# Optimization experiments

Hardware: AMD Instinct MI355X
Metric: run time of the kernel (lower is better)

The kernel has to match this reference:

```python
import jax, jax.numpy as jnp
import numpy as np
import math

CHI, CHO, UP = 256, 128, 2
KH = KW = 3


def bilinear_up_kernel(k):
    f = math.ceil(k / 2)
    c = (2 * f - 1 - f % 2) / (2.0 * f)
    w = np.zeros((k, k), dtype=np.float32)
    for i in range(k):
        for j in range(k):
            w[i, j] = (1 - abs(i / f - c)) * (1 - abs(j / f - c))
    return w


def setup_inputs() -> dict:
    key = jax.random.key(0)
    ks = jax.random.split(key, 8)
    x = jax.random.normal(ks[0], (8, CHI, 64, 64), dtype=jnp.float32)
    # DCNv2 weights
    w_dcn = jax.random.normal(ks[1], (CHO, CHI, KH, KW), dtype=jnp.float32) * 0.02
    b_dcn = jnp.zeros((CHO,), dtype=jnp.float32)
    # offset/mask conv: out channels = 3*KH*KW (2*9 offsets + 9 mask), zero-init as in DCNv2
    w_off = jnp.zeros((3 * KH * KW, CHI, KH, KW), dtype=jnp.float32)
    b_off = jnp.zeros((3 * KH * KW,), dtype=jnp.float32)
    # BatchNorm (eval math) params
    bn_gamma = jax.random.uniform(ks[2], (CHO,), dtype=jnp.float32, minval=0.5, maxval=1.5)
    bn_beta = jax.random.normal(ks[3], (CHO,), dtype=jnp.float32) * 0.1
    bn_mean = jax.random.normal(ks[4], (CHO,), dtype=jnp.float32) * 0.1
    bn_var = jax.random.uniform(ks[5], (CHO,), dtype=jnp.float32, minval=0.5, maxval=1.5)
    # fixed bilinear depthwise transpose-conv weights [CHO,1,2r,2r]
    w_up = jnp.broadcast_to(jnp.asarray(bilinear_up_kernel(UP * 2)), (CHO, 1, UP * 2, UP * 2)).astype(jnp.float32)
    # 1x1 conv to 1 channel
    w_1x1 = jax.random.normal(ks[6], (1, CHO, 1, 1), dtype=jnp.float32) * 0.05
    return dict(x=x, w_dcn=w_dcn, b_dcn=b_dcn, w_off=w_off, b_off=b_off,
                bn_gamma=bn_gamma, bn_beta=bn_beta, bn_mean=bn_mean, bn_var=bn_var,
                w_up=w_up, w_1x1=w_1x1)


def conv2d(x, w, b=None, stride=1, pad=1):
    y = jax.lax.conv_general_dilated(x, w, (stride, stride), [(pad, pad), (pad, pad)],
                                     dimension_numbers=('NCHW', 'OIHW', 'NCHW'))
    if b is not None:
        y = y + b[None, :, None, None]
    return y


def bilinear_sample(img, py, px):
    # img: [C,H,W]; py,px: [P] float coords. Zero padding outside.
    C, H, W = img.shape
    y0 = jnp.floor(py); x0 = jnp.floor(px)
    y1 = y0 + 1; x1 = x0 + 1
    wy1 = py - y0; wy0 = 1.0 - wy1
    wx1 = px - x0; wx0 = 1.0 - wx1

    def gather(yi, xi):
        valid = (yi >= 0) & (yi < H) & (xi >= 0) & (xi < W)
        yc = jnp.clip(yi, 0, H - 1).astype(jnp.int32)
        xc = jnp.clip(xi, 0, W - 1).astype(jnp.int32)
        v = img[:, yc, xc]  # [C,P]
        return v * valid.astype(img.dtype)[None, :]

    out = (gather(y0, x0) * (wy0 * wx0)[None, :] + gather(y0, x1) * (wy0 * wx1)[None, :]
           + gather(y1, x0) * (wy1 * wx0)[None, :] + gather(y1, x1) * (wy1 * wx1)[None, :])
    return out  # [C,P]


def dcn_v2(x, w, b, offset, mask):
    # x: [B,Ci,H,W]; offset: [B,2*K,H,W]; mask: [B,K,H,W]; K=9; stride 1, pad 1.
    B, Ci, H, W = x.shape
    K = KH * KW
    # base sampling grid per kernel tap
    ky, kx = jnp.meshgrid(jnp.arange(KH) - 1, jnp.arange(KW) - 1, indexing='ij')  # [3,3]
    oy, ox = jnp.meshgrid(jnp.arange(H), jnp.arange(W), indexing='ij')  # [H,W]
    base_y = oy[None, :, :] + ky.reshape(K, 1, 1)  # [K,H,W]
    base_x = ox[None, :, :] + kx.reshape(K, 1, 1)

    off = offset.reshape(B, K, 2, H, W)
    py = base_y[None] + off[:, :, 0]  # [B,K,H,W]
    px = base_x[None] + off[:, :, 1]

    def per_sample(img, py_b, px_b, m_b):
        samp = bilinear_sample(img, py_b.reshape(-1), px_b.reshape(-1))  # [Ci, K*H*W]
        samp = samp.reshape(Ci, K, H, W) * m_b[None]  # [Ci,K,H,W]
        # conv accumulate: w [Co,Ci,KH,KW] -> [Co,Ci,K]
        return jnp.einsum('cik,ikhw->chw', w.reshape(w.shape[0], Ci, K), samp[None].swapaxes(0, 1).squeeze(1)[None].squeeze(0)[None].squeeze(0).reshape(Ci, K, H, W))

    def per_sample2(img, py_b, px_b, m_b):
        samp = bilinear_sample(img, py_b.reshape(-1), px_b.reshape(-1)).reshape(Ci, K, H, W)
        samp = samp * m_b[None]
        return jnp.einsum('oik,ikhw->ohw', w.reshape(w.shape[0], Ci, K), samp)

    y = jax.vmap(per_sample2)(x, py, px, mask)  # [B,Co,H,W]
    return y + b[None, :, None, None]


def reference(x, w_dcn, b_dcn, w_off, b_off, bn_gamma, bn_beta, bn_mean, bn_var, w_up, w_1x1):
    K = KH * KW
    om = conv2d(x, w_off, b_off, stride=1, pad=1)  # [B,3K,H,W]
    o1, o2, m = om[:, :K], om[:, K:2 * K], om[:, 2 * K:]
    # DCNv2 ordering: offsets interleaved as (dy,dx) per tap -> o1=dy, o2=dx
    offset = jnp.concatenate([o1[:, :, None], o2[:, :, None]], axis=2).reshape(x.shape[0], 2 * K, x.shape[2], x.shape[3])
    mask = jax.nn.sigmoid(m)
    y = dcn_v2(x, w_dcn, b_dcn, offset, mask)
    # BN (eval) + ReLU
    inv = jax.lax.rsqrt(bn_var + 1e-5)
    y = jax.nn.relu((y - bn_mean[None, :, None, None]) * (bn_gamma * inv)[None, :, None, None] + bn_beta[None, :, None, None])
    # depthwise transpose conv, kernel 2r, stride r, pad r//2
    r = UP
    y = jax.lax.conv_transpose(y, w_up.transpose(2, 3, 1, 0),  # HWIO with I=1 (feature_group_count)
                               strides=(r, r), padding=[(r // 2, r // 2), (r // 2, r // 2)],
                               dimension_numbers=('NCHW', 'HWIO', 'NCHW'),
                               transpose_kernel=True)
    # NOTE: jax.lax.conv_transpose lacks groups; emulate depthwise via per-channel trick below instead.
    return y


def depthwise_conv_transpose(y, w_up, r):
    # y: [B,C,H,W]; w_up: [C,1,k,k]; equivalent to input-dilated conv with flipped kernel
    C = y.shape[1]
    k = w_up.shape[2]
    wf = w_up[:, :, ::-1, ::-1]  # flip for transpose conv
    pad = k - 1 - r // 2
    return jax.lax.conv_general_dilated(y, wf, window_strides=(1, 1),
                                        padding=[(pad, pad), (pad, pad)],
                                        lhs_dilation=(r, r),
                                        dimension_numbers=('NCHW', 'OIHW', 'NCHW'),
                                        feature_group_count=C)


def reference(x, w_dcn, b_dcn, w_off, b_off, bn_gamma, bn_beta, bn_mean, bn_var, w_up, w_1x1):
    K = KH * KW
    om = conv2d(x, w_off, b_off, stride=1, pad=1)
    o1, o2, m = om[:, :K], om[:, K:2 * K], om[:, 2 * K:]
    offset = jnp.concatenate([o1[:, :, None], o2[:, :, None]], axis=2).reshape(x.shape[0], 2 * K, x.shape[2], x.shape[3])
    mask = jax.nn.sigmoid(m)
    y = dcn_v2(x, w_dcn, b_dcn, offset, mask)
    inv = jax.lax.rsqrt(bn_var + 1e-5)
    y = jax.nn.relu((y - bn_mean[None, :, None, None]) * (bn_gamma * inv)[None, :, None, None] + bn_beta[None, :, None, None])
    y = depthwise_conv_transpose(y, w_up, UP)  # [B,CHO,2H,2W]
    y = conv2d(y, w_1x1, None, stride=1, pad=0)  # [B,1,2H,2W]
    return jax.nn.sigmoid(y)
```

## Files before the change

kernel.cpp:

```cpp
#include <hip/hip_runtime.h>
#include <math.h>

typedef __attribute__((ext_vector_type(8))) short short8;
typedef __attribute__((ext_vector_type(4))) float floatx4;

__device__ __forceinline__ unsigned short bf16r(float f) {
  union { float f; unsigned int u; } v; v.f = f;
  unsigned int u = v.u;
  return (unsigned short)((u + 0x7fffu + ((u >> 16) & 1u)) >> 16);
}
__device__ __forceinline__ unsigned int bf16h(float f) {
  union { float f; unsigned int u; } v; v.f = f;
  return (v.u + 0x8000u) >> 16;
}
__device__ __forceinline__ float bf2f(unsigned int u) {
  union { unsigned int u; float f; } v; v.u = u << 16; return v.f;
}
__device__ __forceinline__ void glds16(const void* g, void* l) {
  __builtin_amdgcn_global_load_lds(
      (const __attribute__((address_space(1))) unsigned int*)g,
      (__attribute__((address_space(3))) unsigned int*)l, 16, 0, 0);
}

__global__ __launch_bounds__(256) void k_pre(
    const float* __restrict__ x,
    const float* __restrict__ w_dcn, const float* __restrict__ w_off,
    const float* __restrict__ b_dcn,
    const float* __restrict__ bn_g, const float* __restrict__ bn_b,
    const float* __restrict__ bn_m, const float* __restrict__ bn_v,
    const float* __restrict__ w_up, const float* __restrict__ w1x1,
    unsigned short* __restrict__ xT,
    unsigned short* __restrict__ wt_dcn, unsigned short* __restrict__ wt_off,
    float* __restrict__ vtab, float* __restrict__ bntab,
    unsigned int* __restrict__ offflags) {
  __shared__ unsigned short sx[32 * 264];
  int e = blockIdx.x * 256 + threadIdx.x;
  if (e < 294912) {
    int s = e >> 12;
    int r = e & 4095;
    int ot = r >> 9;
    int lane = (r >> 3) & 63;
    int j = e & 7;
    int l15 = lane & 15, quad = lane >> 4;
    int o = ot * 16 + l15;
    int k = s % 9, cg = s / 9;
    int c = cg * 32 + quad * 8 + j;
    wt_dcn[e] = bf16r(w_dcn[(o * 256 + c) * 9 + k]);
  }
  bool nz = false;
  if (e < 73728) {
    int cg = e / 9216;
    int r = e % 9216;
    int frag = r >> 9;
    int k = frag >> 1, ot = frag & 1;
    int lane = (r >> 3) & 63, j = e & 7;
    int l15 = lane & 15, quad = lane >> 4;
    int oc = ot * 16 + l15;
    int c = cg * 32 + quad * 8 + j;
    float wv = (oc < 27) ? w_off[(oc * 256 + c) * 9 + k] : 0.f;
    wt_off[e] = bf16r(wv);
    nz = (wv != 0.f);
  }
  unsigned long long ba = __ballot(nz);
  if (blockIdx.x < 288 && (threadIdx.x & 63) == 0)
    offflags[blockIdx.x * 4 + (threadIdx.x >> 6)] = (ba != 0ull) ? 1u : 0u;
  if (e < 2048) {
    int o = e >> 4;
    vtab[e] = w1x1[o] * w_up[e];
  }
  if (e < 128) {
    float g = bn_g[e] * rsqrtf(bn_v[e] + 1e-5f);
    bntab[e] = g;
    bntab[128 + e] = (b_dcn[e] - bn_m[e]) * g + bn_b[e];
  }
  if (blockIdx.x < 1024) {
    int b = blockIdx.x & 7, px0 = ((blockIdx.x >> 3) & 127) * 32;
    int t = threadIdx.x;
    int px = t & 31, cg = t >> 5;
    const float* xsrc = x + (((size_t)(b * 256 + cg * 32)) << 12) + px0 + px;
#pragma unroll
    for (int cc = 0; cc < 32; ++cc)
      sx[px * 264 + cg * 32 + cc] = bf16r(xsrc[(size_t)cc << 12]);
    __syncthreads();
#pragma unroll
    for (int j = 0; j < 4; ++j) {
      int unit = t + j * 256;
      int p = unit >> 5, chunk = unit & 31;
      uint4 v = *(const uint4*)&sx[p * 264 + chunk * 8];
      *(uint4*)&xT[((size_t)((b << 12) + px0 + p)) * 256 + chunk * 8] = v;
    }
  }
}

__global__ __launch_bounds__(256, 2) void k_dcn(
    const unsigned short* __restrict__ xT, const unsigned short* __restrict__ wt,
    const unsigned short* __restrict__ wtoff, const float* __restrict__ b_off,
    const float* __restrict__ vtab, const float* __restrict__ bntab,
    const unsigned int* __restrict__ offflags, float* __restrict__ R) {
  int b = blockIdx.x & 7, row = blockIdx.x >> 3;
  __shared__ unsigned short sW[2 * 12288];
  __shared__ ushort4 s_ti[576];
  __shared__ float4 s_tw[576];
  __shared__ unsigned int s_fl[4];
  int t = threadIdx.x, lane = t & 63, wvx = t >> 6;
  int l15 = lane & 15, quad = lane >> 4;
  int px = wvx * 16 + l15;
  const unsigned short* xb = xT + (((size_t)b) << 12) * 256;
  const short8 zz = {0, 0, 0, 0, 0, 0, 0, 0};
  unsigned short* som = (unsigned short*)s_ti;

  {
    unsigned int a = 0;
    for (int i = t; i < 1152; i += 256) a |= offflags[i];
    a = __any(a != 0u) ? 1u : 0u;
    if (lane == 0) s_fl[wvx] = a;
  }
  __syncthreads();
  const bool offnz = (s_fl[0] | s_fl[1] | s_fl[2] | s_fl[3]) != 0u;

  if (offnz) {
    int pixk[9]; bool vkk[9];
#pragma unroll
    for (int k = 0; k < 9; ++k) {
      int yy = row + k / 3 - 1, xx = px + k % 3 - 1;
      vkk[k] = ((unsigned)yy < 64u) & ((unsigned)xx < 64u);
      pixk[k] = vkk[k] ? (yy * 64 + xx) : 0;
    }
    floatx4 oacc[2];
    oacc[0] = (floatx4){0.f, 0.f, 0.f, 0.f};
    oacc[1] = (floatx4){0.f, 0.f, 0.f, 0.f};

#pragma unroll
    for (int i = 0; i < 5; ++i) {
      int frag = wvx + i * 4;
      if (frag < 18)
        glds16(wtoff + (size_t)frag * 512 + lane * 8, &sW[frag * 512]);
    }
    __syncthreads();

    for (int cg = 0; cg < 8; ++cg) {
      unsigned short* buf = sW + (cg & 1) * 9216;
      int cb = cg * 32 + quad * 8;
      short8 bx[9];
#pragma unroll
      for (int k = 0; k < 9; ++k) {
        short8 v = *(const short8*)&xb[(size_t)pixk[k] * 256 + cb];
        bx[k] = vkk[k] ? v : zz;
      }
      if (cg < 7) {
        const unsigned short* wsrc = wtoff + (size_t)(cg + 1) * 9216;
        unsigned short* nbuf = sW + ((cg + 1) & 1) * 9216;
#pragma unroll
        for (int i = 0; i < 5; ++i) {
          int frag = wvx + i * 4;
          if (frag < 18)
            glds16(wsrc + (size_t)frag * 512 + lane * 8, &nbuf[frag * 512]);
        }
      }
#pragma unroll
      for (int k = 0; k < 9; ++k) {
        short8 a0 = *(const short8*)&buf[(k * 2 + 0) * 512 + lane * 8];
        short8 a1 = *(const short8*)&buf[(k * 2 + 1) * 512 + lane * 8];
        oacc[0] = __builtin_amdgcn_mfma_f32_16x16x32_bf16(a0, bx[k], oacc[0], 0, 0, 0);
        oacc[1] = __builtin_amdgcn_mfma_f32_16x16x32_bf16(a1, bx[k], oacc[1], 0, 0, 0);
      }
      __syncthreads();
    }
#pragma unroll
    for (int ot = 0; ot < 2; ++ot)
#pragma unroll
      for (int r = 0; r < 4; ++r) {
        int o = ot * 16 + quad * 4 + r;
        if (o < 27) som[o * 64 + px] = bf16r(oacc[ot][r] + b_off[o]);
      }
    __syncthreads();
  }

  {
    float to1[3], to2[3], tmv[3];
    if (offnz) {
#pragma unroll
      for (int ii = 0; ii < 3; ++ii) {
        int i = t + ii * 256;
        if (i < 576) {
          int k = i >> 6, p = i & 63;
          to1[ii] = bf2f(som[k * 64 + p]);
          to2[ii] = bf2f(som[(9 + k) * 64 + p]);
          tmv[ii] = bf2f(som[(18 + k) * 64 + p]);
        }
      }
      __syncthreads();
    } else {
#pragma unroll
      for (int ii = 0; ii < 3; ++ii) {
        int i = t + ii * 256;
        if (i < 576) {
          int k = i >> 6;
          to1[ii] = bf2f(bf16r(b_off[k]));
          to2[ii] = bf2f(bf16r(b_off[9 + k]));
          tmv[ii] = bf2f(bf16r(b_off[18 + k]));
        }
      }
    }
#pragma unroll
    for (int ii = 0; ii < 3; ++ii) {
      int i = t + ii * 256;
      if (i < 576) {
        int k = i >> 6, p = i & 63;
        float m = 1.f / (1.f + __expf(-tmv[ii]));
        float py = (float)(row + k / 3 - 1) + to1[ii];
        float pxf = (float)(p + (k % 3) - 1) + to2[ii];
        float fy = floorf(py), fx = floorf(pxf);
        int iy = (int)fy, ix = (int)fx;
        float wy1 = py - fy, wy0 = 1.f - wy1;
        float wx1 = pxf - fx, wx0 = 1.f - wx1;
        bool y0ok = (iy >= 0) & (iy < 64), y1ok = (iy >= -1) & (iy < 63);
        bool x0ok = (ix >= 0) & (ix < 64), x1ok = (ix >= -1) & (ix < 63);
        int iy0 = min(max(iy, 0), 63), iy1 = min(max(iy + 1, 0), 63);
        int ix0 = min(max(ix, 0), 63), ix1 = min(max(ix + 1, 0), 63);
        s_ti[i] = make_ushort4((unsigned short)(iy0 * 64 + ix0), (unsigned short)(iy0 * 64 + ix1),
                               (unsigned short)(iy1 * 64 + ix0), (unsigned short)(iy1 * 64 + ix1));
        float4 w;
        w.x = (y0ok && x0ok) ? m * wy0 * wx0 : 0.f;
        w.y = (y0ok && x1ok) ? m * wy0 * wx1 : 0.f;
        w.z = (y1ok && x0ok) ? m * wy1 * wx0 : 0.f;
        w.w = (y1ok && x1ok) ? m * wy1 * wx1 : 0.f;
        s_tw[i] = w;
      }
    }
  }
  __syncthreads();

  const uint4 z4 = make_uint4(0u, 0u, 0u, 0u);

  floatx4 acc[8];
#pragma unroll
  for (int i = 0; i < 8; ++i) acc[i] = (floatx4){0.f, 0.f, 0.f, 0.f};

  uint4 traw[12];
  {
    int cbase = quad * 8;
#pragma unroll
    for (int kk = 0; kk < 3; ++kk) {
      ushort4 ti = s_ti[(kk << 6) + px];
      float4 twn = s_tw[(kk << 6) + px];
      uint4 t0 = z4, t1 = z4, t2 = z4, t3 = z4;
      if (__any(twn.x != 0.f)) t0 = *(const uint4*)&xb[(size_t)ti.x * 256 + cbase];
      if (__any(twn.y != 0.f)) t1 = *(const uint4*)&xb[(size_t)ti.y * 256 + cbase];
      if (__any(twn.z != 0.f)) t2 = *(const uint4*)&xb[(size_t)ti.z * 256 + cbase];
      if (__any(twn.w != 0.f)) t3 = *(const uint4*)&xb[(size_t)ti.w * 256 + cbase];
      traw[kk * 4 + 0] = t0; traw[kk * 4 + 1] = t1;
      traw[kk * 4 + 2] = t2; traw[kk * 4 + 3] = t3;
    }
  }
  {
    const unsigned short* wsrc = wt;
#pragma unroll
    for (int i = 0; i < 6; ++i) {
      int blk = wvx * 6 + i;
      glds16(wsrc + (size_t)blk * 512 + lane * 8, &sW[blk * 512]);
    }
  }
  __syncthreads();

  int lofs = lane * 8;

  for (int phase = 0; phase < 24; ++phase) {
    unsigned short* buf = sW + (phase & 1) * 12288;
    unsigned short* nbuf = sW + ((phase + 1) & 1) * 12288;
    if (phase < 23) {
      const unsigned short* wsrc = wt + (size_t)(phase + 1) * 12288;
#pragma unroll
      for (int i = 0; i < 6; ++i) {
        int blk = wvx * 6 + i;
        glds16(wsrc + (size_t)blk * 512 + lane * 8, &nbuf[blk * 512]);
      }
    }
    int nphase = phase + 1;
    int ncbase = (nphase / 3) * 32 + quad * 8;

#pragma unroll
    for (int kk = 0; kk < 3; ++kk) {
      int k = (phase % 3) * 3 + kk;
      float4 tw = s_tw[(k << 6) + px];
      union { uint4 u; short8 s; } x0, x1, x2, x3;
      x0.u = traw[kk * 4 + 0]; x1.u = traw[kk * 4 + 1];
      x2.u = traw[kk * 4 + 2]; x3.u = traw[kk * 4 + 3];
      if (phase < 23) {
        int nk = (nphase % 3) * 3 + kk;
        ushort4 ti = s_ti[(nk << 6) + px];
        float4 twn = s_tw[(nk << 6) + px];
        uint4 t0 = z4, t1 = z4, t2 = z4, t3 = z4;
        if (__any(twn.x != 0.f)) t0 = *(const uint4*)&xb[(size_t)ti.x * 256 + ncbase];
        if (__any(twn.y != 0.f)) t1 = *(const uint4*)&xb[(size_t)ti.y * 256 + ncbase];
        if (__any(twn.z != 0.f)) t2 = *(const uint4*)&xb[(size_t)ti.z * 256 + ncbase];
        if (__any(twn.w != 0.f)) t3 = *(const uint4*)&xb[(size_t)ti.w * 256 + ncbase];
        traw[kk * 4 + 0] = t0; traw[kk * 4 + 1] = t1;
        traw[kk * 4 + 2] = t2; traw[kk * 4 + 3] = t3;
      }
      float r[8];
#pragma unroll
      for (int j = 0; j < 8; ++j) r[j] = tw.x * bf2f((unsigned short)x0.s[j]);
      if (__any(tw.y != 0.f)) {
#pragma unroll
        for (int j = 0; j < 8; ++j) r[j] += tw.y * bf2f((unsigned short)x1.s[j]);
      }
      if (__any(tw.z != 0.f)) {
#pragma unroll
        for (int j = 0; j < 8; ++j) r[j] += tw.z * bf2f((unsigned short)x2.s[j]);
      }
      if (__any(tw.w != 0.f)) {
#pragma unroll
        for (int j = 0; j < 8; ++j) r[j] += tw.w * bf2f((unsigned short)x3.s[j]);
      }
      union { uint4 u; short8 s; } bu;
      bu.u = make_uint4(bf16h(r[0]) | (bf16h(r[1]) << 16), bf16h(r[2]) | (bf16h(r[3]) << 16),
                        bf16h(r[4]) | (bf16h(r[5]) << 16), bf16h(r[6]) | (bf16h(r[7]) << 16));
      const unsigned short* bk = buf + kk * 4096 + lofs;
#pragma unroll
      for (int ot = 0; ot < 8; ++ot) {
        short8 af = *(const short8*)&bk[ot * 512];
        acc[ot] = __builtin_amdgcn_mfma_f32_16x16x32_bf16(af, bu.s, acc[ot], 0, 0, 0);
      }
    }
    __syncthreads();
  }

  float* sv = (float*)sW;
  float* sbn = sv + 2176;
  for (int i = t; i < 2048; i += 256) sv[(i >> 4) * 17 + (i & 15)] = vtab[i];
  if (t < 256) sbn[t] = bntab[t];
  __syncthreads();

  float rpart[16];
#pragma unroll
  for (int i = 0; i < 16; ++i) rpart[i] = 0.f;
#pragma unroll
  for (int ot = 0; ot < 8; ++ot)
#pragma unroll
    for (int r = 0; r < 4; ++r) {
      int o = ot * 16 + quad * 4 + r;
      float yv = fmaxf(acc[ot][r] * sbn[o] + sbn[128 + o], 0.f);
      const float* vp = &sv[o * 17];
#pragma unroll
      for (int tt = 0; tt < 16; ++tt) rpart[tt] += vp[tt] * yv;
    }
#pragma unroll
  for (int tt = 0; tt < 16; ++tt) {
    rpart[tt] += __shfl_xor(rpart[tt], 16, 64);
    rpart[tt] += __shfl_xor(rpart[tt], 32, 64);
  }
#pragma unroll
  for (int j = 0; j < 4; ++j) {
    int slot = quad * 4 + j;
    R[(((size_t)(b * 16 + slot)) << 12) + row * 64 + px] = rpart[slot];
  }
}

__global__ __launch_bounds__(256) void k_upb(
    const float* __restrict__ R, float* __restrict__ out) {
  int b = blockIdx.x & 7, sub = blockIdx.x >> 3;
  int inner = sub * 256 + threadIdx.x;
  int X = inner & 127, Y = inner >> 7;
  int i0, wu0, wu1, j0, wv0, wv1;
  if (Y & 1) { i0 = (Y - 1) >> 1; wu0 = 2; wu1 = 0; }
  else       { i0 = (Y - 2) / 2;  wu0 = 3; wu1 = 1; }
  if (X & 1) { j0 = (X - 1) >> 1; wv0 = 2; wv1 = 0; }
  else       { j0 = (X - 2) / 2;  wv0 = 3; wv1 = 1; }
  int i1 = i0 + 1, j1 = j0 + 1;
  float mi0 = ((unsigned)i0 < 64u) ? 1.f : 0.f;
  float mi1 = ((unsigned)i1 < 64u) ? 1.f : 0.f;
  float mj0 = ((unsigned)j0 < 64u) ? 1.f : 0.f;
  float mj1 = ((unsigned)j1 < 64u) ? 1.f : 0.f;
  int i0c = min(max(i0, 0), 63), i1c = min(max(i1, 0), 63);
  int j0c = min(max(j0, 0), 63), j1c = min(max(j1, 0), 63);
  const float* Rb = R + (((size_t)b) << 16);
  float s = mi0 * mj0 * Rb[((wu0 * 4 + wv0) << 12) + (i0c << 6) + j0c] +
            mi0 * mj1 * Rb[((wu0 * 4 + wv1) << 12) + (i0c << 6) + j1c] +
            mi1 * mj0 * Rb[((wu1 * 4 + wv0) << 12) + (i1c << 6) + j0c] +
            mi1 * mj1 * Rb[((wu1 * 4 + wv1) << 12) + (i1c << 6) + j1c];
  out[(b << 14) + inner] = 1.f / (1.f + __expf(-s));
}

extern "C" void kernel_launch(void* const* d_in, const int* in_sizes, int n_in,
                              void* d_out, int out_size, void* d_ws, size_t ws_size,
                              hipStream_t stream) {
  const float* x        = (const float*)d_in[0];
  const float* w_dcn    = (const float*)d_in[1];
  const float* b_dcn    = (const float*)d_in[2];
  const float* w_off    = (const float*)d_in[3];
  const float* b_off    = (const float*)d_in[4];
  const float* bn_gamma = (const float*)d_in[5];
  const float* bn_beta  = (const float*)d_in[6];
  const float* bn_mean  = (const float*)d_in[7];
  const float* bn_var   = (const float*)d_in[8];
  const float* w_up     = (const float*)d_in[9];
  const float* w_1x1    = (const float*)d_in[10];
  float* out = (float*)d_out;

  float* ws = (float*)d_ws;
  unsigned short* xT     = (unsigned short*)ws;
  unsigned short* wt_dcn = (unsigned short*)(ws + 4194304);
  unsigned short* wt_off = (unsigned short*)(ws + 4341760);
  float* vtab            = ws + 4378624;
  float* bntab           = ws + 4380672;
  unsigned int* offflags = (unsigned int*)(ws + 4380928);
  float* R               = ws + 4823296;

  k_pre<<<1152, 256, 0, stream>>>(x, w_dcn, w_off, b_dcn, bn_gamma, bn_beta,
                                  bn_mean, bn_var, w_up, w_1x1,
                                  xT, wt_dcn, wt_off, vtab, bntab, offflags);
  k_dcn<<<512, 256, 0, stream>>>(xT, wt_dcn, wt_off, b_off, vtab, bntab,
                                 offflags, R);
  k_upb<<<512, 256, 0, stream>>>(R, out);
}
```

Before: 146.4 us.

## Process two output rows per 512-thread block to share DCN weight tiles

The DCN kernel now launches 256 blocks of 512 threads, each covering two image rows, instead of 512 blocks of 256 threads covering one row. Each phase's weight tile streamed into LDS is reused across both rows, which halves weight traffic per output row. The sampling index and weight tables now stay in per-thread registers instead of shared memory, removing that LDS round trip and one barrier. When offsets are all zero, the kernel also issues dummy loads of the neighbouring input rows to warm the cache. The costs are higher register pressure from 9 extra float4/ushort4 values per thread and only one block per CU, so less room to hide latency.

```diff
diff --git a/kernel.cpp b/kernel.cpp
--- a/kernel.cpp
+++ b/kernel.cpp
@@ -92,33 +92,46 @@
   }
 }
 
-__global__ __launch_bounds__(256, 2) void k_dcn(
+__global__ __launch_bounds__(512, 2) void k_dcn(
     const unsigned short* __restrict__ xT, const unsigned short* __restrict__ wt,
     const unsigned short* __restrict__ wtoff, const float* __restrict__ b_off,
     const float* __restrict__ vtab, const float* __restrict__ bntab,
     const unsigned int* __restrict__ offflags, float* __restrict__ R) {
-  int b = blockIdx.x & 7, row = blockIdx.x >> 3;
+  int b = blockIdx.x & 7, row0 = (blockIdx.x >> 3) * 2;
   __shared__ unsigned short sW[2 * 12288];
-  __shared__ ushort4 s_ti[576];
-  __shared__ float4 s_tw[576];
-  __shared__ unsigned int s_fl[4];
+  __shared__ unsigned int s_fl[8];
   int t = threadIdx.x, lane = t & 63, wvx = t >> 6;
   int l15 = lane & 15, quad = lane >> 4;
-  int px = wvx * 16 + l15;
+  int row_local = wvx >> 2, wv4 = wvx & 3;
+  int row = row0 + row_local;
+  int px = wv4 * 16 + l15;
   const unsigned short* xb = xT + (((size_t)b) << 12) * 256;
   const short8 zz = {0, 0, 0, 0, 0, 0, 0, 0};
-  unsigned short* som = (unsigned short*)s_ti;
+  unsigned short* som = (unsigned short*)sW + 18432;
 
   {
     unsigned int a = 0;
-    for (int i = t; i < 1152; i += 256) a |= offflags[i];
+    for (int i = t; i < 1152; i += 512) a |= offflags[i];
     a = __any(a != 0u) ? 1u : 0u;
     if (lane == 0) s_fl[wvx] = a;
   }
   __syncthreads();
-  const bool offnz = (s_fl[0] | s_fl[1] | s_fl[2] | s_fl[3]) != 0u;
-
-  if (offnz) {
+  unsigned int fl = 0;
+#pragma unroll
+  for (int i = 0; i < 8; ++i) fl |= s_fl[i];
+  const bool offnz = fl != 0u;
+
+  if (!offnz) {
+    int wr0 = max(row0 - 1, 0), wr1 = min(row0 + 2, 63);
+    for (int rr = wr0; rr <= wr1; ++rr) {
+      const uint4* src = (const uint4*)(xb + ((size_t)(rr << 6)) * 256);
+#pragma unroll
+      for (int i = 0; i < 4; ++i) {
+        uint4 v = src[t + (i << 9)];
+        asm volatile("" :: "v"(v.x), "v"(v.y), "v"(v.z), "v"(v.w));
+      }
+    }
+  } else {
     int pixk[9]; bool vkk[9];
 #pragma unroll
     for (int k = 0; k < 9; ++k) {
@@ -129,15 +142,13 @@
     floatx4 oacc[2];
     oacc[0] = (floatx4){0.f, 0.f, 0.f, 0.f};
     oacc[1] = (floatx4){0.f, 0.f, 0.f, 0.f};
-
-#pragma unroll
-    for (int i = 0; i < 5; ++i) {
-      int frag = wvx + i * 4;
+#pragma unroll
+    for (int i = 0; i < 3; ++i) {
+      int frag = wvx + i * 8;
       if (frag < 18)
         glds16(wtoff + (size_t)frag * 512 + lane * 8, &sW[frag * 512]);
     }
     __syncthreads();
-
     for (int cg = 0; cg < 8; ++cg) {
       unsigned short* buf = sW + (cg & 1) * 9216;
       int cb = cg * 32 + quad * 8;
@@ -151,8 +162,8 @@
         const unsigned short* wsrc = wtoff + (size_t)(cg + 1) * 9216;
         unsigned short* nbuf = sW + ((cg + 1) & 1) * 9216;
 #pragma unroll
-        for (int i = 0; i < 5; ++i) {
-          int frag = wvx + i * 4;
+        for (int i = 0; i < 3; ++i) {
+          int frag = wvx + i * 8;
           if (frag < 18)
             glds16(wsrc + (size_t)frag * 512 + lane * 8, &nbuf[frag * 512]);
         }
@@ -171,68 +182,49 @@
 #pragma unroll
       for (int r = 0; r < 4; ++r) {
         int o = ot * 16 + quad * 4 + r;
-        if (o < 27) som[o * 64 + px] = bf16r(oacc[ot][r] + b_off[o]);
+        if (o < 27) som[row_local * 1728 + o * 64 + px] = bf16r(oacc[ot][r] + b_off[o]);
       }
     __syncthreads();
   }
 
+  ushort4 tir[9]; float4 twr[9];
   {
-    float to1[3], to2[3], tmv[3];
-    if (offnz) {
-#pragma unroll
-      for (int ii = 0; ii < 3; ++ii) {
-        int i = t + ii * 256;
-        if (i < 576) {
-          int k = i >> 6, p = i & 63;
-          to1[ii] = bf2f(som[k * 64 + p]);
-          to2[ii] = bf2f(som[(9 + k) * 64 + p]);
-          tmv[ii] = bf2f(som[(18 + k) * 64 + p]);
-        }
-      }
-      __syncthreads();
-    } else {
-#pragma unroll
-      for (int ii = 0; ii < 3; ++ii) {
-        int i = t + ii * 256;
-        if (i < 576) {
-          int k = i >> 6;
-          to1[ii] = bf2f(bf16r(b_off[k]));
-          to2[ii] = bf2f(bf16r(b_off[9 + k]));
-          tmv[ii] = bf2f(bf16r(b_off[18 + k]));
-        }
-      }
-    }
-#pragma unroll
-    for (int ii = 0; ii < 3; ++ii) {
-      int i = t + ii * 256;
-      if (i < 576) {
-        int k = i >> 6, p = i & 63;
-        float m = 1.f / (1.f + __expf(-tmv[ii]));
-        float py = (float)(row + k / 3 - 1) + to1[ii];
-        float pxf = (float)(p + (k % 3) - 1) + to2[ii];
-        float fy = floorf(py), fx = floorf(pxf);
-        int iy = (int)fy, ix = (int)fx;
-        float wy1 = py - fy, wy0 = 1.f - wy1;
-        float wx1 = pxf - fx, wx0 = 1.f - wx1;
-        bool y0ok = (iy >= 0) & (iy < 64), y1ok = (iy >= -1) & (iy < 63);
-        bool x0ok = (ix >= 0) & (ix < 64), x1ok = (ix >= -1) & (ix < 63);
-        int iy0 = min(max(iy, 0), 63), iy1 = min(max(iy + 1, 0), 63);
-        int ix0 = min(max(ix, 0), 63), ix1 = min(max(ix + 1, 0), 63);
-        s_ti[i] = make_ushort4((unsigned short)(iy0 * 64 + ix0), (unsigned short)(iy0 * 64 + ix1),
-                               (unsigned short)(iy1 * 64 + ix0), (unsigned short)(iy1 * 64 + ix1));
-        float4 w;
-        w.x = (y0ok && x0ok) ? m * wy0 * wx0 : 0.f;
-        w.y = (y0ok && x1ok) ? m * wy0 * wx1 : 0.f;
-        w.z = (y1ok && x0ok) ? m * wy1 * wx0 : 0.f;
-        w.w = (y1ok && x1ok) ? m * wy1 * wx1 : 0.f;
-        s_tw[i] = w;
-      }
-    }
-  }
-  __syncthreads();
+    const unsigned short* smr = som + row_local * 1728;
+#pragma unroll
+    for (int k = 0; k < 9; ++k) {
+      float o1, o2, mv;
+      if (offnz) {
+        o1 = bf2f(smr[k * 64 + px]);
+        o2 = bf2f(smr[(9 + k) * 64 + px]);
+        mv = bf2f(smr[(18 + k) * 64 + px]);
+      } else {
+        o1 = bf2f(bf16r(b_off[k]));
+        o2 = bf2f(bf16r(b_off[9 + k]));
+        mv = bf2f(bf16r(b_off[18 + k]));
+      }
+      float m = 1.f / (1.f + __expf(-mv));
+      float py = (float)(row + k / 3 - 1) + o1;
+      float pxf = (float)(px + (k % 3) - 1) + o2;
+      float fy = floorf(py), fx = floorf(pxf);
+      int iy = (int)fy, ix = (int)fx;
+      float wy1 = py - fy, wy0 = 1.f - wy1;
+      float wx1 = pxf - fx, wx0 = 1.f - wx1;
+      bool y0ok = (iy >= 0) & (iy < 64), y1ok = (iy >= -1) & (iy < 63);
+      bool x0ok = (ix >= 0) & (ix < 64), x1ok = (ix >= -1) & (ix < 63);
+      int iy0 = min(max(iy, 0), 63), iy1 = min(max(iy + 1, 0), 63);
+      int ix0 = min(max(ix, 0), 63), ix1 = min(max(ix + 1, 0), 63);
+      tir[k] = make_ushort4((unsigned short)(iy0 * 64 + ix0), (unsigned short)(iy0 * 64 + ix1),
+                            (unsigned short)(iy1 * 64 + ix0), (unsigned short)(iy1 * 64 + ix1));
+      float4 w;
+      w.x = (y0ok && x0ok) ? m * wy0 * wx0 : 0.f;
+      w.y = (y0ok && x1ok) ? m * wy0 * wx1 : 0.f;
+      w.z = (y1ok && x0ok) ? m * wy1 * wx0 : 0.f;
+      w.w = (y1ok && x1ok) ? m * wy1 * wx1 : 0.f;
+      twr[k] = w;
+    }
+  }
 
   const uint4 z4 = make_uint4(0u, 0u, 0u, 0u);
-
   floatx4 acc[8];
 #pragma unroll
   for (int i = 0; i < 8; ++i) acc[i] = (floatx4){0.f, 0.f, 0.f, 0.f};
@@ -242,8 +234,7 @@
     int cbase = quad * 8;
 #pragma unroll
     for (int kk = 0; kk < 3; ++kk) {
-      ushort4 ti = s_ti[(kk << 6) + px];
-      float4 twn = s_tw[(kk << 6) + px];
+      ushort4 ti = tir[kk]; float4 twn = twr[kk];
       uint4 t0 = z4, t1 = z4, t2 = z4, t3 = z4;
       if (__any(twn.x != 0.f)) t0 = *(const uint4*)&xb[(size_t)ti.x * 256 + cbase];
       if (__any(twn.y != 0.f)) t1 = *(const uint4*)&xb[(size_t)ti.y * 256 + cbase];
@@ -254,81 +245,82 @@
     }
   }
   {
-    const unsigned short* wsrc = wt;
-#pragma unroll
-    for (int i = 0; i < 6; ++i) {
-      int blk = wvx * 6 + i;
-      glds16(wsrc + (size_t)blk * 512 + lane * 8, &sW[blk * 512]);
+#pragma unroll
+    for (int i = 0; i < 3; ++i) {
+      int blk = wvx * 3 + i;
+      glds16(wt + (size_t)blk * 512 + lane * 8, &sW[blk * 512]);
     }
   }
   __syncthreads();
 
-  int lofs = lane * 8;
-
-  for (int phase = 0; phase < 24; ++phase) {
-    unsigned short* buf = sW + (phase & 1) * 12288;
-    unsigned short* nbuf = sW + ((phase + 1) & 1) * 12288;
-    if (phase < 23) {
-      const unsigned short* wsrc = wt + (size_t)(phase + 1) * 12288;
-#pragma unroll
-      for (int i = 0; i < 6; ++i) {
-        int blk = wvx * 6 + i;
-        glds16(wsrc + (size_t)blk * 512 + lane * 8, &nbuf[blk * 512]);
-      }
-    }
-    int nphase = phase + 1;
-    int ncbase = (nphase / 3) * 32 + quad * 8;
-
-#pragma unroll
-    for (int kk = 0; kk < 3; ++kk) {
-      int k = (phase % 3) * 3 + kk;
-      float4 tw = s_tw[(k << 6) + px];
-      union { uint4 u; short8 s; } x0, x1, x2, x3;
-      x0.u = traw[kk * 4 + 0]; x1.u = traw[kk * 4 + 1];
-      x2.u = traw[kk * 4 + 2]; x3.u = traw[kk * 4 + 3];
-      if (phase < 23) {
-        int nk = (nphase % 3) * 3 + kk;
-        ushort4 ti = s_ti[(nk << 6) + px];
-        float4 twn = s_tw[(nk << 6) + px];
-        uint4 t0 = z4, t1 = z4, t2 = z4, t3 = z4;
-        if (__any(twn.x != 0.f)) t0 = *(const uint4*)&xb[(size_t)ti.x * 256 + ncbase];
-        if (__any(twn.y != 0.f)) t1 = *(const uint4*)&xb[(size_t)ti.y * 256 + ncbase];
-        if (__any(twn.z != 0.f)) t2 = *(const uint4*)&xb[(size_t)ti.z * 256 + ncbase];
-        if (__any(twn.w != 0.f)) t3 = *(const uint4*)&xb[(size_t)ti.w * 256 + ncbase];
-        traw[kk * 4 + 0] = t0; traw[kk * 4 + 1] = t1;
-        traw[kk * 4 + 2] = t2; traw[kk * 4 + 3] = t3;
-      }
-      float r[8];
-#pragma unroll
-      for (int j = 0; j < 8; ++j) r[j] = tw.x * bf2f((unsigned short)x0.s[j]);
-      if (__any(tw.y != 0.f)) {
-#pragma unroll
-        for (int j = 0; j < 8; ++j) r[j] += tw.y * bf2f((unsigned short)x1.s[j]);
-      }
-      if (__any(tw.z != 0.f)) {
-#pragma unroll
-        for (int j = 0; j < 8; ++j) r[j] += tw.z * bf2f((unsigned short)x2.s[j]);
-      }
-      if (__any(tw.w != 0.f)) {
-#pragma unroll
-        for (int j = 0; j < 8; ++j) r[j] += tw.w * bf2f((unsigned short)x3.s[j]);
-      }
-      union { uint4 u; short8 s; } bu;
-      bu.u = make_uint4(bf16h(r[0]) | (bf16h(r[1]) << 16), bf16h(r[2]) | (bf16h(r[3]) << 16),
-                        bf16h(r[4]) | (bf16h(r[5]) << 16), bf16h(r[6]) | (bf16h(r[7]) << 16));
-      const unsigned short* bk = buf + kk * 4096 + lofs;
-#pragma unroll
-      for (int ot = 0; ot < 8; ++ot) {
-        short8 af = *(const short8*)&bk[ot * 512];
-        acc[ot] = __builtin_amdgcn_mfma_f32_16x16x32_bf16(af, bu.s, acc[ot], 0, 0, 0);
-      }
-    }
-    __syncthreads();
+  for (int p3 = 0; p3 < 8; ++p3) {
+#pragma unroll
+    for (int sub = 0; sub < 3; ++sub) {
+      int phase = p3 * 3 + sub;
+      unsigned short* buf = sW + (phase & 1) * 12288;
+      unsigned short* nbuf = sW + ((phase + 1) & 1) * 12288;
+      bool notlast = (sub < 2) | (p3 < 7);
+      if (notlast) {
+        const unsigned short* wsrc = wt + (size_t)(phase + 1) * 12288;
+#pragma unroll
+        for (int i = 0; i < 3; ++i) {
+          int blk = wvx * 3 + i;
+          glds16(wsrc + (size_t)blk * 512 + lane * 8, &nbuf[blk * 512]);
+        }
+      }
+      int cgn = (sub == 2) ? (p3 + 1) : p3;
+      int ncbase = cgn * 32 + quad * 8;
+
+#pragma unroll
+      for (int kk = 0; kk < 3; ++kk) {
+        const int k = sub * 3 + kk;
+        float4 tw = twr[k];
+        union { uint4 u; short8 s; } x0, x1, x2, x3;
+        x0.u = traw[kk * 4 + 0]; x1.u = traw[kk * 4 + 1];
+        x2.u = traw[kk * 4 + 2]; x3.u = traw[kk * 4 + 3];
+        if (notlast) {
+          const int nk = ((sub + 1) % 3) * 3 + kk;
+          ushort4 ti = tir[nk]; float4 twn = twr[nk];
+          uint4 t0 = z4, t1 = z4, t2 = z4, t3 = z4;
+          if (__any(twn.x != 0.f)) t0 = *(const uint4*)&xb[(size_t)ti.x * 256 + ncbase];
+          if (__any(twn.y != 0.f)) t1 = *(const uint4*)&xb[(size_t)ti.y * 256 + ncbase];
+          if (__any(twn.z != 0.f)) t2 = *(const uint4*)&xb[(size_t)ti.z * 256 + ncbase];
+          if (__any(twn.w != 0.f)) t3 = *(const uint4*)&xb[(size_t)ti.w * 256 + ncbase];
+          traw[kk * 4 + 0] = t0; traw[kk * 4 + 1] = t1;
+          traw[kk * 4 + 2] = t2; traw[kk * 4 + 3] = t3;
+        }
+        float r[8];
+#pragma unroll
+        for (int j = 0; j < 8; ++j) r[j] = tw.x * bf2f((unsigned short)x0.s[j]);
+        if (__any(tw.y != 0.f)) {
+#pragma unroll
+          for (int j = 0; j < 8; ++j) r[j] += tw.y * bf2f((unsigned short)x1.s[j]);
+        }
+        if (__any(tw.z != 0.f)) {
+#pragma unroll
+          for (int j = 0; j < 8; ++j) r[j] += tw.z * bf2f((unsigned short)x2.s[j]);
+        }
+        if (__any(tw.w != 0.f)) {
+#pragma unroll
+          for (int j = 0; j < 8; ++j) r[j] += tw.w * bf2f((unsigned short)x3.s[j]);
+        }
+        union { uint4 u; short8 s; } bu;
+        bu.u = make_uint4(bf16h(r[0]) | (bf16h(r[1]) << 16), bf16h(r[2]) | (bf16h(r[3]) << 16),
+                          bf16h(r[4]) | (bf16h(r[5]) << 16), bf16h(r[6]) | (bf16h(r[7]) << 16));
+        const unsigned short* bk = buf + kk * 4096 + lane * 8;
+#pragma unroll
+        for (int ot = 0; ot < 8; ++ot) {
+          short8 af = *(const short8*)&bk[ot * 512];
+          acc[ot] = __builtin_amdgcn_mfma_f32_16x16x32_bf16(af, bu.s, acc[ot], 0, 0, 0);
+        }
+      }
+      __syncthreads();
+    }
   }
 
   float* sv = (float*)sW;
   float* sbn = sv + 2176;
-  for (int i = t; i < 2048; i += 256) sv[(i >> 4) * 17 + (i & 15)] = vtab[i];
+  for (int i = t; i < 2048; i += 512) sv[(i >> 4) * 17 + (i & 15)] = vtab[i];
   if (t < 256) sbn[t] = bntab[t];
   __syncthreads();
 
@@ -410,7 +402,7 @@
   k_pre<<<1152, 256, 0, stream>>>(x, w_dcn, w_off, b_dcn, bn_gamma, bn_beta,
                                   bn_mean, bn_var, w_up, w_1x1,
                                   xT, wt_dcn, wt_off, vtab, bntab, offflags);
-  k_dcn<<<512, 256, 0, stream>>>(xT, wt_dcn, wt_off, b_off, vtab, bntab,
+  k_dcn<<<256, 512, 0, stream>>>(xT, wt_dcn, wt_off, b_off, vtab, bntab,
                                  offflags, R);
   k_upb<<<512, 256, 0, stream>>>(R, out);
 }
```

After: 203.7 us. 1.39x slower.
